# Performance work log

Measured on AMD Instinct MI355X. Metric: run time of the kernel, lower is better.

Reference implementation:

```python
import jax, jax.numpy as jnp
import numpy as np

HID = 256
VOCAB = 1000
REPEAT = 32
ALPHA = 1.0
LBR = 0.2
THRESH = 0.8 * ALPHA * (1.0 - LBR)  # 0.64


def _lstm_layer(x, Wih, Whh, bih, bhh):
    # x: [B,S,D]; returns hidden states [S,B,H] (torch gate order i,f,g,o)
    B = x.shape[0]
    H = Whh.shape[1]
    xg = jnp.einsum('bsd,gd->sbg', x, Wih) + (bih + bhh)  # [S,B,4H]
    def step(carry, gx):
        h, c = carry
        g = gx + h @ Whh.T
        i, f, gg, o = jnp.split(g, 4, axis=-1)
        c = jax.nn.sigmoid(f) * c + jax.nn.sigmoid(i) * jnp.tanh(gg)
        h = jax.nn.sigmoid(o) * jnp.tanh(c)
        return (h, c), h
    init = (jnp.zeros((B, H), x.dtype), jnp.zeros((B, H), x.dtype))
    _, hs = jax.lax.scan(step, init, xg)
    return hs


def _encode(x, Wih0, Whh0, bih0, bhh0, Wih1, Whh1, bih1, bhh1):
    # 2-layer LSTM (dropout inactive at inference), then sum over time -> [B,H]
    hs = _lstm_layer(x, Wih0, Whh0, bih0, bhh0)                      # [S,B,H]
    hs = _lstm_layer(jnp.transpose(hs, (1, 0, 2)), Wih1, Whh1, bih1, bhh1)
    return hs.sum(0)


def setup_inputs():
    key = jax.random.key(0)
    ks = jax.random.split(key, 20)
    B, S, D, H, P = 64, 128, 64, HID, 1024
    s = jnp.float32(0.05)
    return {
        'x1': jax.random.normal(ks[0], (B, S, D), jnp.float32),
        'x2': jax.random.normal(ks[1], (B, S, D), jnp.float32),
        'Wih0': s * jax.random.normal(ks[2], (4 * H, D), jnp.float32),
        'Whh0': s * jax.random.normal(ks[3], (4 * H, H), jnp.float32),
        'bih0': s * jax.random.normal(ks[4], (4 * H,), jnp.float32),
        'bhh0': s * jax.random.normal(ks[5], (4 * H,), jnp.float32),
        'Wih1': s * jax.random.normal(ks[6], (4 * H, H), jnp.float32),
        'Whh1': s * jax.random.normal(ks[7], (4 * H, H), jnp.float32),
        'bih1': s * jax.random.normal(ks[8], (4 * H,), jnp.float32),
        'bhh1': s * jax.random.normal(ks[9], (4 * H,), jnp.float32),
        'fc1_w': s * jax.random.normal(ks[10], (P, 2 * H), jnp.float32),
        'fc1_b': s * jax.random.normal(ks[11], (P,), jnp.float32),
        'fc2_w': s * jax.random.normal(ks[12], (P, P), jnp.float32),
        'fc2_b': s * jax.random.normal(ks[13], (P,), jnp.float32),
        'fc3_w': s * jax.random.normal(ks[14], (VOCAB * REPEAT, P), jnp.float32),
        'fc3_b': s * jax.random.normal(ks[15], (VOCAB * REPEAT,), jnp.float32),
        'bn_g': jnp.ones((P,), jnp.float32),
        'bn_b': jnp.zeros((P,), jnp.float32),
    }


def reference(x1, x2, Wih0, Whh0, bih0, bhh0, Wih1, Whh1, bih1, bhh1,
              fc1_w, fc1_b, fc2_w, fc2_b, fc3_w, fc3_b, bn_g, bn_b):
    out1 = _encode(x1, Wih0, Whh0, bih0, bhh0, Wih1, Whh1, bih1, bhh1)
    out2 = _encode(x2, Wih0, Whh0, bih0, bhh0, Wih1, Whh1, bih1, bhh1)
    h = jnp.concatenate([out1, out2], axis=1)                # [B,2H]
    h = jax.nn.gelu(h @ fc1_w.T + fc1_b, approximate=False)  # exact gelu (torch)
    h = h + jax.nn.relu(h @ fc2_w.T + fc2_b)
    # BatchNorm1d with batch statistics (training-mode normalization)
    mu = h.mean(0)
    var = h.var(0)
    h = (h - mu) / jnp.sqrt(var + 1e-5) * bn_g + bn_b
    scores = jax.nn.relu(h @ fc3_w.T + fc3_b)
    scores = scores.reshape(-1, VOCAB, REPEAT)               # [B,V,R]
    # vectorized replacement of the per-row .item() selection loop:
    # number of atoms selected per row at threshold 0.8*alpha*(1-lbr)
    num_select = jnp.maximum(1, (scores > THRESH).sum(axis=(1, 2)))
    return scores, num_select
```

## Files before the change

### kernel.cpp

```cpp
#include <hip/hip_runtime.h>
#include <cmath>


typedef _Float16 f16;
typedef _Float16 f16x8 __attribute__((ext_vector_type(8)));
typedef _Float16 f16x4 __attribute__((ext_vector_type(4)));
typedef float f32x4 __attribute__((ext_vector_type(4)));

#define MFMA(a,b,c) __builtin_amdgcn_mfma_f32_16x16x32_f16((a),(b),(c),0,0,0)
#define LSTR 280
#define FPAD 32

__device__ __forceinline__ float frcp(float x) { return __builtin_amdgcn_rcpf(x); }
__device__ __forceinline__ float sigf(float x)  { return frcp(1.f + __expf(-x)); }
__device__ __forceinline__ float tanhf_(float x){ return 1.f - 2.f*frcp(__expf(2.f*x) + 1.f); }

__device__ __forceinline__ void wait_flag(int* f, int target) {
    while (__hip_atomic_load(f, __ATOMIC_RELAXED, __HIP_MEMORY_SCOPE_AGENT) < target)
        __builtin_amdgcn_s_sleep(1);
    (void)__hip_atomic_load(f, __ATOMIC_ACQUIRE, __HIP_MEMORY_SCOPE_AGENT);
}

__global__ void k_convert(const float* __restrict__ Wih0, const float* __restrict__ Whh0,
                          const float* __restrict__ bih0, const float* __restrict__ bhh0,
                          const float* __restrict__ Wih1, const float* __restrict__ Whh1,
                          const float* __restrict__ bih1, const float* __restrict__ bhh1,
                          f16* __restrict__ w16, float* __restrict__ bsum,
                          int* __restrict__ flg)
{
    int i = blockIdx.x * 256 + threadIdx.x;
    if (i < 65536)  w16[i] = (f16)Wih0[i];
    if (i < 262144) {
        w16[65536  + i] = (f16)Whh0[i];
        w16[327680 + i] = (f16)Wih1[i];
        w16[589824 + i] = (f16)Whh1[i];
    }
    if (i < 1024) { bsum[i] = bih0[i] + bhh0[i]; bsum[1024 + i] = bih1[i] + bhh1[i]; }
    if (i < 16*FPAD) flg[i] = 0;
}

template<int K, bool CVT>
__global__ __launch_bounds__(512)
void k_proj(const void* __restrict__ A0v, const void* __restrict__ A1v,
            const f16* __restrict__ Bw, const float* __restrict__ bias,
            f16* __restrict__ out)
{
    const int w = threadIdx.x >> 6, lane = threadIdx.x & 63;
    const int quad = lane >> 4, l16 = lane & 15;
    const long m0 = (long)blockIdx.x * 128 + w * 16;
    f32x4 acc[2][4] = {};
    #pragma unroll
    for (int kc = 0; kc < K/32; ++kc) {
        const int ko = kc*32 + quad*8;
        f16x8 a;
        if (CVT) {
            const float* Af = (const float*)((m0 < 8192) ? A0v : A1v);
            const float* ap = Af + ((m0 & 8191) + l16)*K + ko;
            float4 v0 = *(const float4*)ap, v1 = *(const float4*)(ap + 4);
            a[0]=(f16)v0.x; a[1]=(f16)v0.y; a[2]=(f16)v0.z; a[3]=(f16)v0.w;
            a[4]=(f16)v1.x; a[5]=(f16)v1.y; a[6]=(f16)v1.z; a[7]=(f16)v1.w;
        } else {
            a = *(const f16x8*)((const f16*)A0v + (m0 + l16)*K + ko);
        }
        #pragma unroll
        for (int tg = 0; tg < 2; ++tg) {
            const int ti = blockIdx.y*2 + tg;
            #pragma unroll
            for (int g = 0; g < 4; ++g) {
                f16x8 b = *(const f16x8*)(Bw + (long)(g*256 + ti*16 + l16)*K + ko);
                acc[tg][g] = MFMA(a, b, acc[tg][g]);
            }
        }
    }
    #pragma unroll
    for (int tg = 0; tg < 2; ++tg) {
        const int ti = blockIdx.y*2 + tg;
        float bi[4];
        #pragma unroll
        for (int g = 0; g < 4; ++g) bi[g] = bias[g*256 + ti*16 + l16];
        #pragma unroll
        for (int r = 0; r < 4; ++r) {
            long mm = m0 + quad*4 + r;
            f16x4 pv;
            #pragma unroll
            for (int g = 0; g < 4; ++g) pv[g] = (f16)(acc[tg][g][r] + bi[g]);
            *(f16x4*)(out + mm*1024 + ti*64 + l16*4) = pv;
        }
    }
}

__global__ __launch_bounds__(512, 2)
void k_mega(const f16* __restrict__ w16, const f16* __restrict__ xg0,
            f16* __restrict__ xg1, f16* __restrict__ h0s,
            const float* __restrict__ bsum1, float* __restrict__ out_enc,
            int* __restrict__ flags)
{
    __shared__ f16 wl[256*LSTR];
    __shared__ f16 hb[2*16*LSTR];
    const int tid = threadIdx.x;
    const int w = tid >> 6, lane = tid & 63;
    const int quad = lane >> 4, l16 = lane & 15;
    const int role = blockIdx.x >> 3, g = blockIdx.x & 7;
    int* fl_h0  = flags + g*FPAD;
    int* fl_xg1 = flags + (8+g)*FPAD;

    const f16* W = (role == 0) ? w16 + 65536
                 : (role == 1) ? w16 + 327680
                               : w16 + 589824;

    f16x8 bres[6][8];
    #pragma unroll
    for (int s6 = 0; s6 < 6; ++s6) {
        const int tile = (s6 >> 1)*16 + 2*w + (s6 & 1);
        #pragma unroll
        for (int kc = 0; kc < 8; ++kc)
            bres[s6][kc] = *(const f16x8*)(W + (tile*16 + l16)*256 + kc*32 + quad*8);
    }
    {
        const int r = tid >> 1, hh = tid & 1;
        const f16* src = W + (768 + r)*256 + hh*128;
        f16* dst = wl + r*LSTR + hh*128;
        #pragma unroll
        for (int j = 0; j < 16; ++j)
            *(f16x8*)(dst + j*8) = *(const f16x8*)(src + j*8);
    }

    if (role == 1) {
        float bi[2][4];
        #pragma unroll
        for (int q = 0; q < 2; ++q)
            #pragma unroll
            for (int g4 = 0; g4 < 4; ++g4) bi[q][g4] = bsum1[g4*256 + (2*w+q)*16 + l16];
        __syncthreads();
        #pragma unroll 1
        for (int s = 0; s < 128; ++s) {
            if ((s & 1) == 0) {
                if (tid == 0) wait_flag(fl_h0, s + 2);
                __syncthreads();
            }
            const f16* hrow = h0s + ((long)s*128 + g*16 + l16)*256 + quad*8;
            f16x8 av[8];
            #pragma unroll
            for (int kc = 0; kc < 8; ++kc) av[kc] = *(const f16x8*)(hrow + kc*32);
            #pragma unroll
            for (int q = 0; q < 2; ++q) {
                const int ti = 2*w + q;
                f32x4 ai = {}, af = {}, ag = {}, ao = {};
                #pragma unroll
                for (int kc = 0; kc < 8; ++kc) {
                    f16x8 bo = *(const f16x8*)(wl + (ti*16 + l16)*LSTR + kc*32 + quad*8);
                    ai = MFMA(av[kc], bres[q][kc],   ai);
                    af = MFMA(av[kc], bres[2+q][kc], af);
                    ag = MFMA(av[kc], bres[4+q][kc], ag);
                    ao = MFMA(av[kc], bo,            ao);
                }
                #pragma unroll
                for (int r = 0; r < 4; ++r) {
                    f16x4 pv;
                    pv[0] = (f16)(ai[r] + bi[q][0]);
                    pv[1] = (f16)(af[r] + bi[q][1]);
                    pv[2] = (f16)(ag[r] + bi[q][2]);
                    pv[3] = (f16)(ao[r] + bi[q][3]);
                    *(f16x4*)(xg1 + ((long)(g*16 + quad*4 + r)*128 + s)*1024
                                  + ti*64 + l16*4) = pv;
                }
            }
            if (s & 1) {
                __syncthreads();
                if (tid == 0)
                    __hip_atomic_store(fl_xg1, s + 1, __ATOMIC_RELEASE,
                                       __HIP_MEMORY_SCOPE_AGENT);
            }
        }
        return;
    }

    for (int i = tid; i < 2*16*LSTR; i += 512) hb[i] = (f16)0.f;

    const f16* xg = (role == 0) ? xg0 : xg1;
    const f16* xp[4];
    #pragma unroll
    for (int r = 0; r < 4; ++r)
        xp[r] = xg + (long)(g*16 + quad*4 + r)*131072 + (2*w)*64 + l16*4;

    float c[8]    = {0,0,0,0,0,0,0,0};
    float oacc[8] = {0,0,0,0,0,0,0,0};
    __syncthreads();

    #pragma unroll 1
    for (int s = 0; s < 128; ++s) {
        const int rb = s & 1, wb = rb ^ 1;
        if (role == 2 && (s & 1) == 0) {
            if (tid == 0) wait_flag(fl_xg1, s + 2);
            __syncthreads();
        }
        if (role == 0 && s > 0) {
            const int cc = tid >> 5, kk = (tid & 31) * 8;
            f16x8 hv = *(const f16x8*)(hb + (rb*16 + cc)*LSTR + kk);
            *(f16x8*)(h0s + ((long)(s-1)*128 + g*16 + cc)*256 + kk) = hv;
        }
        f16x4 xv[2][4];
        #pragma unroll
        for (int r = 0; r < 4; ++r) {
            xv[0][r] = *(const f16x4*)(xp[r]);
            xv[1][r] = *(const f16x4*)(xp[r] + 64);
        }
        #pragma unroll
        for (int q = 0; q < 2; ++q) {
            const int ti = 2*w + q;
            f32x4 ai = {}, af = {}, ag = {}, ao = {};
            #pragma unroll
            for (int kc = 0; kc < 8; ++kc) {
                f16x8 a  = *(const f16x8*)(hb + (rb*16 + l16)*LSTR + kc*32 + quad*8);
                f16x8 bo = *(const f16x8*)(wl + (ti*16 + l16)*LSTR + kc*32 + quad*8);
                ai = MFMA(a, bres[q][kc],   ai);
                af = MFMA(a, bres[2+q][kc], af);
                ag = MFMA(a, bres[4+q][kc], ag);
                ao = MFMA(a, bo,            ao);
            }
            #pragma unroll
            for (int r = 0; r < 4; ++r) {
                float gi = sigf(ai[r] + (float)xv[q][r][0]);
                float gf = sigf(af[r] + (float)xv[q][r][1]);
                float gg = tanhf_(ag[r] + (float)xv[q][r][2]);
                float go = sigf(ao[r] + (float)xv[q][r][3]);
                const int ci = q*4 + r;
                float cn = gf*c[ci] + gi*gg;
                c[ci] = cn;
                float hn = go * tanhf_(cn);
                if (role == 2) oacc[ci] += hn;
                hb[(wb*16 + quad*4 + r)*LSTR + ti*16 + l16] = (f16)hn;
            }
        }
        #pragma unroll
        for (int r = 0; r < 4; ++r) xp[r] += 1024;
        __syncthreads();
        if (role == 0 && (s & 1) == 0 && s > 0 && tid == 0)
            __hip_atomic_store(fl_h0, s, __ATOMIC_RELEASE,
                               __HIP_MEMORY_SCOPE_AGENT);
    }
    if (role == 0) {
        const int cc = tid >> 5, kk = (tid & 31) * 8;
        f16x8 hv = *(const f16x8*)(hb + (0*16 + cc)*LSTR + kk);
        *(f16x8*)(h0s + ((long)127*128 + g*16 + cc)*256 + kk) = hv;
        __syncthreads();
        if (tid == 0)
            __hip_atomic_store(fl_h0, 128, __ATOMIC_RELEASE,
                               __HIP_MEMORY_SCOPE_AGENT);
    }
    if (role == 2) {
        #pragma unroll
        for (int q = 0; q < 2; ++q)
            #pragma unroll
            for (int r = 0; r < 4; ++r)
                out_enc[(long)(g*16 + quad*4 + r)*256 + (2*w+q)*16 + l16] = oacc[q*4 + r];
    }
}

template<int K, int MODE>
__global__ __launch_bounds__(256)
void k_fc(const float* __restrict__ A, const float* __restrict__ W,
          const float* __restrict__ bias, const float* __restrict__ res,
          const float* __restrict__ bng, const float* __restrict__ bnb,
          float* __restrict__ out, const int Nst)
{
    __shared__ float ws[32*64];
    __shared__ float as[64*64];
    __shared__ float mus[32], rss[32];
    const int tid = threadIdx.x;
    const int n0 = blockIdx.x * 32;
    const int m2 = tid & 31, ndg = tid >> 5;
    float acc[2][4] = {};
    for (int kc = 0; kc < K/64; ++kc) {
        __syncthreads();
        {
            const int col = tid >> 3, k8 = (tid & 7)*8;
            const float* src = W + (long)(n0 + col)*K + kc*64 + k8;
            *(float4*)(ws + col*64 + k8)     = *(const float4*)(src);
            *(float4*)(ws + col*64 + k8 + 4) = *(const float4*)(src + 4);
        }
        {
            const int m = tid >> 2, j4 = (tid & 3)*16;
            #pragma unroll
            for (int i4 = 0; i4 < 4; ++i4) {
                const int kk = kc*64 + j4 + i4*4;
                const float* srcA;
                if (MODE == 0) srcA = (kk < 256) ? (A + (long)m*256 + kk)
                                                 : (A + 16384 + (long)m*256 + kk - 256);
                else           srcA = A + (long)m*K + kk;
                float4 v = *(const float4*)srcA;
                as[(j4 + i4*4 + 0)*64 + m] = v.x;
                as[(j4 + i4*4 + 1)*64 + m] = v.y;
                as[(j4 + i4*4 + 2)*64 + m] = v.z;
                as[(j4 + i4*4 + 3)*64 + m] = v.w;
            }
        }
        __syncthreads();
        #pragma unroll 4
        for (int k4 = 0; k4 < 64; k4 += 4) {
            float a0[4], a1[4];
            #pragma unroll
            for (int i = 0; i < 4; ++i) {
                a0[i] = as[(k4+i)*64 + m2];
                a1[i] = as[(k4+i)*64 + m2 + 32];
            }
            #pragma unroll
            for (int j = 0; j < 4; ++j) {
                const float4 wv = *(const float4*)(ws + (ndg*4 + j)*64 + k4);
                acc[0][j] += a0[0]*wv.x + a0[1]*wv.y + a0[2]*wv.z + a0[3]*wv.w;
                acc[1][j] += a1[0]*wv.x + a1[1]*wv.y + a1[2]*wv.z + a1[3]*wv.w;
            }
        }
    }
    if (MODE == 1) {
        float vv[2][4];
        #pragma unroll
        for (int i = 0; i < 2; ++i)
            #pragma unroll
            for (int j = 0; j < 4; ++j) {
                const int m = m2 + i*32, nn = n0 + ndg*4 + j;
                vv[i][j] = res[(long)m*1024 + nn] + fmaxf(acc[i][j] + bias[nn], 0.f);
            }
        __syncthreads();
        #pragma unroll
        for (int i = 0; i < 2; ++i)
            #pragma unroll
            for (int j = 0; j < 4; ++j)
                as[(m2 + i*32)*33 + ndg*4 + j] = vv[i][j];
        __syncthreads();
        if (tid < 32) {
            float s = 0.f, ss = 0.f;
            #pragma unroll 4
            for (int m = 0; m < 64; ++m) {
                float x = as[m*33 + tid];
                s += x; ss += x*x;
            }
            const float mu = s * (1.f/64.f);
            mus[tid] = mu;
            rss[tid] = rsqrtf(ss * (1.f/64.f) - mu*mu + 1e-5f);
        }
        __syncthreads();
        #pragma unroll
        for (int i = 0; i < 2; ++i)
            #pragma unroll
            for (int j = 0; j < 4; ++j) {
                const int m = m2 + i*32, cl = ndg*4 + j, nn = n0 + cl;
                out[(long)m*Nst + nn] = (vv[i][j] - mus[cl]) * rss[cl] * bng[nn] + bnb[nn];
            }
        return;
    }
    #pragma unroll
    for (int i = 0; i < 2; ++i) {
        const int m = m2 + i*32;
        #pragma unroll
        for (int j = 0; j < 4; ++j) {
            const int nn = n0 + ndg*4 + j;
            float v = acc[i][j] + bias[nn];
            if (MODE == 0) v = 0.5f * v * (1.0f + erff(v * 0.7071067811865475f));
            else           v = fmaxf(v, 0.f);
            out[(long)m*Nst + nn] = v;
        }
    }
}

__global__ void k_count(const float* __restrict__ scores, float* __restrict__ outc)
{
    const int row = blockIdx.x, tid = threadIdx.x;
    const float* p = scores + (long)row*32000;
    int cnt = 0;
    for (int i = tid; i < 32000; i += 256)
        cnt += ((double)p[i] > 0.6400000000000001) ? 1 : 0;
    __shared__ int red[256];
    red[tid] = cnt; __syncthreads();
    for (int off = 128; off > 0; off >>= 1) {
        if (tid < off) red[tid] += red[tid + off];
        __syncthreads();
    }
    if (tid == 0) outc[row] = (float)(red[0] < 1 ? 1 : red[0]);
}

extern "C" void kernel_launch(void* const* d_in, const int* in_sizes, int n_in,
                              void* d_out, int out_size, void* d_ws, size_t ws_size,
                              hipStream_t stream)
{
    const float* x1    = (const float*)d_in[0];
    const float* x2    = (const float*)d_in[1];
    const float* Wih0  = (const float*)d_in[2];
    const float* Whh0  = (const float*)d_in[3];
    const float* bih0  = (const float*)d_in[4];
    const float* bhh0  = (const float*)d_in[5];
    const float* Wih1  = (const float*)d_in[6];
    const float* Whh1  = (const float*)d_in[7];
    const float* bih1  = (const float*)d_in[8];
    const float* bhh1  = (const float*)d_in[9];
    const float* fc1_w = (const float*)d_in[10];
    const float* fc1_b = (const float*)d_in[11];
    const float* fc2_w = (const float*)d_in[12];
    const float* fc2_b = (const float*)d_in[13];
    const float* fc3_w = (const float*)d_in[14];
    const float* fc3_b = (const float*)d_in[15];
    const float* bn_g  = (const float*)d_in[16];
    const float* bn_b  = (const float*)d_in[17];
    float* out = (float*)d_out;

    char* ws = (char*)d_ws;
    f16*   w16   = (f16*)(ws);
    float* bsum  = (float*)(ws + 1703936);
    int*   flags = (int*)(ws + 1712128);
    float* enc   = (float*)(ws + 1714176);
    f16*   h0s   = (f16*)(ws + 1845248);
    f16*   xg0   = (f16*)(ws + 10233856);
    f16*   xg1   = (f16*)(ws + 43788288);
    float* h1    = (float*)(ws + 10233856);
    float* h3    = (float*)(ws + 10496000);

    k_convert<<<1024, 256, 0, stream>>>(Wih0,Whh0,bih0,bhh0,Wih1,Whh1,bih1,bhh1,
                                        w16, bsum, flags);
    k_proj<64,true><<<dim3(128,8), 512, 0, stream>>>(x1, x2, w16, bsum, xg0);
    k_mega<<<24, 512, 0, stream>>>(w16, xg0, xg1, h0s, bsum + 1024, enc, flags);
    k_fc<512,0><<<32, 256, 0, stream>>>(enc, fc1_w, fc1_b, nullptr, nullptr, nullptr, h1, 1024);
    k_fc<1024,1><<<32, 256, 0, stream>>>(h1, fc2_w, fc2_b, h1, bn_g, bn_b, h3, 1024);
    k_fc<1024,2><<<1000, 256, 0, stream>>>(h3, fc3_w, fc3_b, nullptr, nullptr, nullptr, out, 32000);
    k_count<<<64, 256, 0, stream>>>(out, out + 2048000);
}
```

Measured before the change: 971.6 us.

## Use f16 MFMA for final FC layer with f16 batchnorm output

The batchnorm stage now writes its normalized activations as f16. A new fc3 kernel computes the 32000-wide output layer with 16x16x32 f16 MFMA, converting fp32 weights to f16 in registers as it streams them. The old scalar fp32 shared-memory tile path for fc3 is removed. This trades fp32 accuracy for matrix-core throughput, which could flip values near the 0.64 threshold and change the count.

```diff
diff --git a/kernel.cpp b/kernel.cpp
--- a/kernel.cpp
+++ b/kernel.cpp
@@ -262,7 +262,7 @@
 void k_fc(const float* __restrict__ A, const float* __restrict__ W,
           const float* __restrict__ bias, const float* __restrict__ res,
           const float* __restrict__ bng, const float* __restrict__ bnb,
-          float* __restrict__ out, const int Nst)
+          float* __restrict__ out, f16* __restrict__ out16, const int Nst)
 {
     __shared__ float ws[32*64];
     __shared__ float as[64*64];
@@ -345,7 +345,8 @@
             #pragma unroll
             for (int j = 0; j < 4; ++j) {
                 const int m = m2 + i*32, cl = ndg*4 + j, nn = n0 + cl;
-                out[(long)m*Nst + nn] = (vv[i][j] - mus[cl]) * rss[cl] * bng[nn] + bnb[nn];
+                out16[(long)m*Nst + nn] =
+                    (f16)((vv[i][j] - mus[cl]) * rss[cl] * bng[nn] + bnb[nn]);
             }
         return;
     }
@@ -356,10 +357,41 @@
         for (int j = 0; j < 4; ++j) {
             const int nn = n0 + ndg*4 + j;
             float v = acc[i][j] + bias[nn];
-            if (MODE == 0) v = 0.5f * v * (1.0f + erff(v * 0.7071067811865475f));
-            else           v = fmaxf(v, 0.f);
+            v = 0.5f * v * (1.0f + erff(v * 0.7071067811865475f));
             out[(long)m*Nst + nn] = v;
         }
+    }
+}
+
+__global__ __launch_bounds__(256)
+void k_fc3(const f16* __restrict__ A, const float* __restrict__ W,
+           const float* __restrict__ bias, float* __restrict__ out)
+{
+    const int w = threadIdx.x >> 6, lane = threadIdx.x & 63;
+    const int quad = lane >> 4, l16 = lane & 15;
+    const int m0 = w*16, n0 = blockIdx.x*64;
+    f32x4 acc[4] = {};
+    #pragma unroll 1
+    for (int kc = 0; kc < 32; ++kc) {
+        const int ko = kc*32 + quad*8;
+        f16x8 a = *(const f16x8*)(A + (m0 + l16)*1024 + ko);
+        #pragma unroll
+        for (int nt = 0; nt < 4; ++nt) {
+            const float* wp = W + (long)(n0 + nt*16 + l16)*1024 + ko;
+            float4 v0 = *(const float4*)wp, v1 = *(const float4*)(wp + 4);
+            f16x8 b;
+            b[0]=(f16)v0.x; b[1]=(f16)v0.y; b[2]=(f16)v0.z; b[3]=(f16)v0.w;
+            b[4]=(f16)v1.x; b[5]=(f16)v1.y; b[6]=(f16)v1.z; b[7]=(f16)v1.w;
+            acc[nt] = MFMA(a, b, acc[nt]);
+        }
+    }
+    #pragma unroll
+    for (int nt = 0; nt < 4; ++nt) {
+        const int nn = n0 + nt*16 + l16;
+        const float bi = bias[nn];
+        #pragma unroll
+        for (int r = 0; r < 4; ++r)
+            out[(long)(m0 + quad*4 + r)*32000 + nn] = fmaxf(acc[nt][r] + bi, 0.f);
     }
 }
 
@@ -412,14 +444,16 @@
     f16*   xg0   = (f16*)(ws + 10233856);
     f16*   xg1   = (f16*)(ws + 43788288);
     float* h1    = (float*)(ws + 10233856);
-    float* h3    = (float*)(ws + 10496000);
+    f16*   h3f16 = (f16*)(ws + 10496000);
 
     k_convert<<<1024, 256, 0, stream>>>(Wih0,Whh0,bih0,bhh0,Wih1,Whh1,bih1,bhh1,
                                         w16, bsum, flags);
     k_proj<64,true><<<dim3(128,8), 512, 0, stream>>>(x1, x2, w16, bsum, xg0);
     k_mega<<<24, 512, 0, stream>>>(w16, xg0, xg1, h0s, bsum + 1024, enc, flags);
-    k_fc<512,0><<<32, 256, 0, stream>>>(enc, fc1_w, fc1_b, nullptr, nullptr, nullptr, h1, 1024);
-    k_fc<1024,1><<<32, 256, 0, stream>>>(h1, fc2_w, fc2_b, h1, bn_g, bn_b, h3, 1024);
-    k_fc<1024,2><<<1000, 256, 0, stream>>>(h3, fc3_w, fc3_b, nullptr, nullptr, nullptr, out, 32000);
+    k_fc<512,0><<<32, 256, 0, stream>>>(enc, fc1_w, fc1_b, nullptr, nullptr, nullptr,
+                                        h1, nullptr, 1024);
+    k_fc<1024,1><<<32, 256, 0, stream>>>(h1, fc2_w, fc2_b, h1, bn_g, bn_b,
+                                         nullptr, h3f16, 1024);
+    k_fc3<<<500, 256, 0, stream>>>(h3f16, fc3_w, fc3_b, out);
     k_count<<<64, 256, 0, stream>>>(out, out + 2048000);
 }
```

Measured after the change: 940.8 us. 3.2% less time.
